# Kernel tuning notes

Hardware: AMD Instinct MI355X
Metric: run time of the kernel (lower is better)

## Reference

```python
import jax, jax.numpy as jnp
import numpy as np

N_HEAD = 16
D_HEAD = 64
D_MODEL = 1024
D_INNER = 4096
QLEN = 1024
MLEN = 1024
BSZ = 2
LN_EPS = 1e-5


def _layer_norm(x, g, b, eps=LN_EPS):
    mu = jnp.mean(x, axis=-1, keepdims=True)
    var = jnp.var(x, axis=-1, keepdims=True)
    return (x - mu) * jax.lax.rsqrt(var + eps) * g + b


def _rel_shift(x):
    # x: [qlen, rlen, bsz, n_head]
    q, r, b, n = x.shape
    zp = jnp.zeros((q, 1, b, n), x.dtype)
    xp = jnp.concatenate([zp, x], axis=1).reshape(r + 1, q, b, n)
    return xp[1:].reshape(q, r, b, n)


def setup_inputs() -> dict:
    key = jax.random.key(0)
    ks = jax.random.split(key, 12)
    klen = MLEN + QLEN
    w = jax.random.normal(ks[0], (QLEN, BSZ, D_MODEL), jnp.float32)
    r = jax.random.normal(ks[1], (klen, D_MODEL), jnp.float32)
    mems = jax.random.normal(ks[2], (MLEN, BSZ, D_MODEL), jnp.float32)
    # causal mask: query i attends keys j <= i + mlen
    i = jnp.arange(QLEN)[:, None]
    j = jnp.arange(klen)[None, :]
    attn_mask = (j > i + MLEN)[:, :, None]  # [qlen, klen, 1] bool
    s = 0.02
    params = dict(
        qkv_w=jax.random.normal(ks[3], (3 * N_HEAD * D_HEAD, D_MODEL), jnp.float32) * s,
        r_net_w=jax.random.normal(ks[4], (N_HEAD * D_HEAD, D_MODEL), jnp.float32) * s,
        o_w=jax.random.normal(ks[5], (D_MODEL, N_HEAD * D_HEAD), jnp.float32) * s,
        r_r_bias=jax.random.normal(ks[6], (N_HEAD, D_HEAD), jnp.float32) * s,
        r_w_bias=jax.random.normal(ks[7], (N_HEAD, D_HEAD), jnp.float32) * s,
        ln1_g=jnp.ones((D_MODEL,), jnp.float32),
        ln1_b=jnp.zeros((D_MODEL,), jnp.float32),
        ff_w1=jax.random.normal(ks[8], (D_INNER, D_MODEL), jnp.float32) * s,
        ff_b1=jnp.zeros((D_INNER,), jnp.float32),
        ff_w2=jax.random.normal(ks[9], (D_MODEL, D_INNER), jnp.float32) * s,
        ff_b2=jnp.zeros((D_MODEL,), jnp.float32),
        ln2_g=jnp.ones((D_MODEL,), jnp.float32),
        ln2_b=jnp.zeros((D_MODEL,), jnp.float32),
    )
    return dict(w=w, r=r, mems=mems, attn_mask=attn_mask, **params)


def reference(w, r, mems, attn_mask, qkv_w, r_net_w, o_w, r_r_bias, r_w_bias,
              ln1_g, ln1_b, ff_w1, ff_b1, ff_w2, ff_b2, ln2_g, ln2_b):
    qlen, bsz = w.shape[0], w.shape[1]
    scale = 1.0 / (D_HEAD ** 0.5)
    cat = jnp.concatenate([mems, w], axis=0)              # [klen, b, d_model]
    klen = cat.shape[0]
    w_heads = cat @ qkv_w.T                                # [klen, b, 3*n*d]
    wq, wk, wv = jnp.split(w_heads, 3, axis=-1)
    wq = wq[-qlen:]
    r_head_k = (r @ r_net_w.T).reshape(-1, N_HEAD, D_HEAD)  # [rlen, n, d]
    wq = wq.reshape(qlen, bsz, N_HEAD, D_HEAD)
    wk = wk.reshape(klen, bsz, N_HEAD, D_HEAD)
    wv = wv.reshape(klen, bsz, N_HEAD, D_HEAD)
    AC = jnp.einsum('ibnd,jbnd->ijbn', wq + r_w_bias, wk)   # content term
    BD = jnp.einsum('ibnd,jnd->ijbn', wq + r_r_bias, r_head_k)
    BD = _rel_shift(BD)                                     # position term
    attn_score = (AC + BD) * scale
    mask_value = jnp.finfo(attn_score.dtype).min
    attn_score = jnp.where(attn_mask[:, :, :, None], mask_value, attn_score)
    attn_prob = jax.nn.softmax(attn_score, axis=1)
    attn_vec = jnp.einsum('ijbn,jbnd->ibnd', attn_prob, wv)
    attn_vec = attn_vec.reshape(qlen, bsz, N_HEAD * D_HEAD)
    attn_out = attn_vec @ o_w.T
    h = _layer_norm(w + attn_out, ln1_g, ln1_b)             # post-lnorm
    core = jax.nn.relu(h @ ff_w1.T + ff_b1) @ ff_w2.T + ff_b2
    out = _layer_norm(h + core, ln2_g, ln2_b)
    return out
```

## Files before the change

kernel.cpp:

```cpp
#include <hip/hip_runtime.h>
#include <math.h>

#define QLEN 1024
#define MLEN 1024
#define KLEN 2048
#define BSZc 2
#define NH 16
#define DH 64
#define DM 1024
#define DI 4096

typedef unsigned short ushort_t;
typedef __attribute__((ext_vector_type(8))) short short8;
typedef __attribute__((ext_vector_type(4))) float f32x4;

__device__ __forceinline__ ushort_t f2bf(float x) {
    unsigned int u = __float_as_uint(x);
    unsigned int r = (u + 0x7FFFu + ((u >> 16) & 1u)) >> 16;
    return (ushort_t)r;
}

__device__ __forceinline__ void gload_lds16(const ushort_t* g, ushort_t* l) {
    __builtin_amdgcn_global_load_lds(
        (const __attribute__((address_space(1))) unsigned int*)g,
        (__attribute__((address_space(3))) unsigned int*)l,
        16, 0, 0);
}

__device__ __forceinline__ void cast8(const float* s, ushort_t* d, int g) {
    const float4 a = *(const float4*)(s + g * 8);
    const float4 b = *(const float4*)(s + g * 8 + 4);
    short8 o;
    o[0] = (short)f2bf(a.x); o[1] = (short)f2bf(a.y);
    o[2] = (short)f2bf(a.z); o[3] = (short)f2bf(a.w);
    o[4] = (short)f2bf(b.x); o[5] = (short)f2bf(b.y);
    o[6] = (short)f2bf(b.z); o[7] = (short)f2bf(b.w);
    *(short8*)(d + g * 8) = o;
}

__global__ __launch_bounds__(256)
void cast_phase1(const float* __restrict__ qkv_w, const float* __restrict__ rnet_w,
                 const float* __restrict__ mems, const float* __restrict__ w,
                 const float* __restrict__ r,
                 ushort_t* __restrict__ W1, ushort_t* __restrict__ W2,
                 ushort_t* __restrict__ Acat, ushort_t* __restrict__ Rsrc)
{
    int g = blockIdx.x * 256 + threadIdx.x;
    if (g < 393216)            { cast8(qkv_w,  W1,              g); }
    else if (g < 524288)       { cast8(rnet_w, W2,              g - 393216); }
    else if (g < 786432)       { cast8(mems,   Acat,            g - 524288); }
    else if (g < 1048576)      { cast8(w,      Acat + 2097152,  g - 786432); }
    else if (g < 1310720)      { cast8(r,      Rsrc,            g - 1048576); }
}

__global__ __launch_bounds__(256)
void cast_phase2(const float* __restrict__ o_w, const float* __restrict__ ffw1,
                 const float* __restrict__ ffw2,
                 ushort_t* __restrict__ W3, ushort_t* __restrict__ W4,
                 ushort_t* __restrict__ W5)
{
    int g = blockIdx.x * 256 + threadIdx.x;
    if (g < 131072)            { cast8(o_w,  W3, g); }
    else if (g < 655360)       { cast8(ffw1, W4, g - 131072); }
    else if (g < 1179648)      { cast8(ffw2, W5, g - 655360); }
}

template<int EMODE, int ACT, int BN, int SPLIT>
__global__ __launch_bounds__(256)
void gemm_mfma(const ushort_t* __restrict__ A, const ushort_t* __restrict__ B,
               const float* __restrict__ bias,
               void* __restrict__ O0v, void* __restrict__ O1v,
               int M, int N, int Ks, int lda, int ldb)
{
    constexpr int JT = BN / 32;
    __shared__ ushort_t At0[128 * 32];
    __shared__ ushort_t At1[128 * 32];
    __shared__ ushort_t Bt0[BN * 32];
    __shared__ ushort_t Bt1[BN * 32];

    const int tid  = threadIdx.x;
    const int lane = tid & 63;
    const int w    = tid >> 6;
    const int lr   = lane & 15;
    const int quad = lane >> 4;
    const int m0   = blockIdx.x * 128;
    const int n0   = blockIdx.y * BN;
    const int z    = (SPLIT > 1) ? (int)blockIdx.z : 0;
    const int kbase = z * Ks;
    const int wm0  = (w >> 1) * 64;
    const int wn0  = (w & 1) * (BN / 2);

    f32x4 acc[4][JT];
#pragma unroll
    for (int it = 0; it < 4; ++it)
#pragma unroll
        for (int jt = 0; jt < JT; ++jt) acc[it][jt] = (f32x4){0.f, 0.f, 0.f, 0.f};

    const int srow = lane >> 2;
    const int scol = (lane & 3) << 3;
    const ushort_t* Ag = A + (size_t)(m0 + w * 32 + srow) * lda + kbase + scol;
    ushort_t* a00 = At0 + (w * 32) * 32;
    ushort_t* a01 = At0 + (w * 32 + 16) * 32;
    ushort_t* a10 = At1 + (w * 32) * 32;
    ushort_t* a11 = At1 + (w * 32 + 16) * 32;
    const ushort_t* Bg;
    ushort_t *b00, *b01 = nullptr, *b10, *b11 = nullptr;
    if (BN == 128) {
        Bg  = B + (size_t)(n0 + w * 32 + srow) * ldb + kbase + scol;
        b00 = Bt0 + (w * 32) * 32;
        b01 = Bt0 + (w * 32 + 16) * 32;
        b10 = Bt1 + (w * 32) * 32;
        b11 = Bt1 + (w * 32 + 16) * 32;
    } else {
        Bg  = B + (size_t)(n0 + w * 16 + srow) * ldb + kbase + scol;
        b00 = Bt0 + (w * 16) * 32;
        b10 = Bt1 + (w * 16) * 32;
    }

    const ushort_t* Ato0 = At0 + (wm0 + lr) * 32 + quad * 8;
    const ushort_t* Ato1 = At1 + (wm0 + lr) * 32 + quad * 8;
    const ushort_t* Bto0 = Bt0 + (wn0 + lr) * 32 + quad * 8;
    const ushort_t* Bto1 = Bt1 + (wn0 + lr) * 32 + quad * 8;

    for (int k0 = 0; k0 < Ks; k0 += 64) {
        __syncthreads();
        gload_lds16(Ag + k0, a00);
        gload_lds16(Ag + (size_t)16 * lda + k0, a01);
        gload_lds16(Ag + k0 + 32, a10);
        gload_lds16(Ag + (size_t)16 * lda + k0 + 32, a11);
        if (BN == 128) {
            gload_lds16(Bg + k0, b00);
            gload_lds16(Bg + (size_t)16 * ldb + k0, b01);
            gload_lds16(Bg + k0 + 32, b10);
            gload_lds16(Bg + (size_t)16 * ldb + k0 + 32, b11);
        } else {
            gload_lds16(Bg + k0, b00);
            gload_lds16(Bg + k0 + 32, b10);
        }
        __syncthreads();

        short8 af[4], bf[JT];
#pragma unroll
        for (int it = 0; it < 4; ++it)
            af[it] = *(const short8*)(Ato0 + it * 16 * 32);
#pragma unroll
        for (int jt = 0; jt < JT; ++jt)
            bf[jt] = *(const short8*)(Bto0 + jt * 16 * 32);
#pragma unroll
        for (int it = 0; it < 4; ++it)
#pragma unroll
            for (int jt = 0; jt < JT; ++jt)
                acc[it][jt] = __builtin_amdgcn_mfma_f32_16x16x32_bf16(
                    af[it], bf[jt], acc[it][jt], 0, 0, 0);
#pragma unroll
        for (int it = 0; it < 4; ++it)
            af[it] = *(const short8*)(Ato1 + it * 16 * 32);
#pragma unroll
        for (int jt = 0; jt < JT; ++jt)
            bf[jt] = *(const short8*)(Bto1 + jt * 16 * 32);
#pragma unroll
        for (int it = 0; it < 4; ++it)
#pragma unroll
            for (int jt = 0; jt < JT; ++jt)
                acc[it][jt] = __builtin_amdgcn_mfma_f32_16x16x32_bf16(
                    af[it], bf[jt], acc[it][jt], 0, 0, 0);
    }

#pragma unroll
    for (int it = 0; it < 4; ++it)
#pragma unroll
        for (int jt = 0; jt < JT; ++jt)
#pragma unroll
            for (int rg = 0; rg < 4; ++rg) {
                const int m = m0 + wm0 + it * 16 + quad * 4 + rg;
                const int n = n0 + wn0 + jt * 16 + lr;
                float v = acc[it][jt][rg];
                if (EMODE == 0) {
                    float* dst = (float*)(z ? O1v : O0v);
                    if (bias && z == 0) v += bias[n];
                    dst[(size_t)m * N + n] = v;
                } else {
                    v += bias[n];
                    if (ACT == 1) v = fmaxf(v, 0.f);
                    ((ushort_t*)O0v)[(size_t)m * N + n] = f2bf(v);
                }
            }
}

__global__ __launch_bounds__(256)
void gemm_qkvr(const ushort_t* __restrict__ Acat, const ushort_t* __restrict__ W1,
               const ushort_t* __restrict__ Rsrc, const ushort_t* __restrict__ W2,
               ushort_t* __restrict__ Qac, ushort_t* __restrict__ Qbd,
               ushort_t* __restrict__ Kbf, ushort_t* __restrict__ Vtb,
               ushort_t* __restrict__ Rh,
               const float* __restrict__ rwb, const float* __restrict__ rrb)
{
    __shared__ ushort_t At[128 * 32];
    __shared__ ushort_t Bt[128 * 32];

    const int bid  = blockIdx.x;
    const bool isr = bid >= 768;
    const ushort_t* A; const ushort_t* B; int m0, n0;
    if (!isr) { A = Acat; B = W1; m0 = (bid & 31) * 128; n0 = (bid >> 5) * 128; }
    else { int t = bid - 768; A = Rsrc; B = W2; m0 = (t & 15) * 128; n0 = (t >> 4) * 128; }
    const int K = 1024;

    const int tid  = threadIdx.x;
    const int lane = tid & 63;
    const int w    = tid >> 6;
    const int lr   = lane & 15;
    const int quad = lane >> 4;
    const int wm0  = (w >> 1) * 64;
    const int wn0  = (w & 1) * 64;

    f32x4 acc[4][4];
#pragma unroll
    for (int it = 0; it < 4; ++it)
#pragma unroll
        for (int jt = 0; jt < 4; ++jt) acc[it][jt] = (f32x4){0.f, 0.f, 0.f, 0.f};

    const int srow = lane >> 2;
    const int scol = (lane & 3) << 3;
    const ushort_t* Ag = A + (size_t)(m0 + w * 32 + srow) * K + scol;
    const ushort_t* Bg = B + (size_t)(n0 + w * 32 + srow) * K + scol;
    ushort_t* lA0 = At + (w * 32) * 32;
    ushort_t* lA1 = At + (w * 32 + 16) * 32;
    ushort_t* lB0 = Bt + (w * 32) * 32;
    ushort_t* lB1 = Bt + (w * 32 + 16) * 32;

    const ushort_t* Ato = At + (wm0 + lr) * 32 + quad * 8;
    const ushort_t* Bto = Bt + (wn0 + lr) * 32 + quad * 8;

    for (int k0 = 0; k0 < K; k0 += 32) {
        __syncthreads();
        gload_lds16(Ag + k0, lA0);
        gload_lds16(Ag + (size_t)16 * K + k0, lA1);
        gload_lds16(Bg + k0, lB0);
        gload_lds16(Bg + (size_t)16 * K + k0, lB1);
        __syncthreads();

        short8 af[4], bf[4];
#pragma unroll
        for (int it = 0; it < 4; ++it)
            af[it] = *(const short8*)(Ato + it * 16 * 32);
#pragma unroll
        for (int jt = 0; jt < 4; ++jt)
            bf[jt] = *(const short8*)(Bto + jt * 16 * 32);
#pragma unroll
        for (int it = 0; it < 4; ++it)
#pragma unroll
            for (int jt = 0; jt < 4; ++jt)
                acc[it][jt] = __builtin_amdgcn_mfma_f32_16x16x32_bf16(
                    af[it], bf[jt], acc[it][jt], 0, 0, 0);
    }

#pragma unroll
    for (int it = 0; it < 4; ++it)
#pragma unroll
        for (int jt = 0; jt < 4; ++jt)
#pragma unroll
            for (int rg = 0; rg < 4; ++rg) {
                const int m = m0 + wm0 + it * 16 + quad * 4 + rg;
                const int n = n0 + wn0 + jt * 16 + lr;
                const float v = acc[it][jt][rg];
                if (!isr) {
                    const int j = m >> 1, b = m & 1;
                    const int part = n >> 10, hh = (n >> 6) & 15, d = n & 63;
                    if (part == 0) {
                        if (j >= MLEN) {
                            const int qi = j - MLEN;
                            const size_t qidx = (((size_t)(b * NH + hh)) * QLEN + qi) * DH + d;
                            Qac[qidx] = f2bf(v + rwb[hh * DH + d]);
                            Qbd[qidx] = f2bf(v + rrb[hh * DH + d]);
                        }
                    } else if (part == 1) {
                        Kbf[(((size_t)(b * NH + hh)) * KLEN + j) * DH + d] = f2bf(v);
                    } else {
                        Vtb[(((size_t)(b * NH + hh)) * DH + d) * KLEN + j] = f2bf(v);
                    }
                } else {
                    const int hh = n >> 6, d = n & 63;
                    Rh[(((size_t)hh) * KLEN + m) * DH + d] = f2bf(v);
                }
            }
}

__global__ __launch_bounds__(256, 4)
void attn_mfma(const ushort_t* __restrict__ Qac, const ushort_t* __restrict__ Qbd,
               const ushort_t* __restrict__ Kb, const ushort_t* __restrict__ Vt,
               const ushort_t* __restrict__ Rb,
               float* __restrict__ Op0, float* __restrict__ Op1,
               float* __restrict__ Mp, float* __restrict__ Lp)
{
    __shared__ ushort_t Rt[128][72];
    __shared__ float    Bw[4][16][84];

    const int tid  = threadIdx.x;
    const int lane = tid & 63;
    const int w    = tid >> 6;
    const int lr   = lane & 15;
    const int quad = lane >> 4;
    const int qt   = blockIdx.x;
    const int s    = blockIdx.y;
    const int bh   = blockIdx.z;
    const int i0   = qt << 6;
    const int h    = bh & 15;
    const int b    = bh >> 4;

    short8 qaf[2], qbf[2];
    {
        const size_t rowoff = ((size_t)bh * QLEN + i0 + w * 16 + lr) * DH;
#pragma unroll
        for (int kt = 0; kt < 2; ++kt) {
            qaf[kt] = *(const short8*)(Qac + rowoff + kt * 32 + quad * 8);
            qbf[kt] = *(const short8*)(Qbd + rowoff + kt * 32 + quad * 8);
        }
    }

    f32x4 O[4];
#pragma unroll
    for (int nt = 0; nt < 4; ++nt) O[nt] = (f32x4){0.f, 0.f, 0.f, 0.f};
    float m_run = -3.4e38f, l_run = 0.f;

    const int nc  = qt + 17;
    const int stw = 3 - w;
    const float SC = 0.125f * 1.44269504f;
    const ushort_t* Kh = Kb + (size_t)bh * KLEN * DH;
    const ushort_t* Vh = Vt + (size_t)bh * DH * KLEN;
    const ushort_t* Rhp = Rb + (size_t)h * KLEN * DH;

    for (int c = s; c < nc; c += 2) {
        const int j0 = c << 6;
        const int wb = 960 - i0 + j0;
        __syncthreads();
#pragma unroll
        for (int t = 0; t < 4; ++t) {
            int f = tid + (t << 8);
            int rl2 = f >> 3, c8 = (f & 7) << 3;
            int g = wb + rl2;
            int gc = g > (KLEN - 1) ? (KLEN - 1) : g;
            *(int4*)&Rt[rl2][c8] = *(const int4*)(Rhp + (size_t)gc * DH + c8);
        }
        __syncthreads();

#pragma unroll
        for (int ctl = 0; ctl < 5; ++ctl) {
            const int wr = (stw + ctl) * 16 + lr;
            f32x4 z = (f32x4){0.f, 0.f, 0.f, 0.f};
#pragma unroll
            for (int kt = 0; kt < 2; ++kt) {
                short8 rb2 = *(const short8*)&Rt[wr][kt * 32 + quad * 8];
                z = __builtin_amdgcn_mfma_f32_16x16x32_bf16(qbf[kt], rb2, z, 0, 0, 0);
            }
#pragma unroll
            for (int rg = 0; rg < 4; ++rg)
                Bw[w][quad * 4 + rg][ctl * 16 + lr] = z[rg];
        }
#pragma unroll
        for (int ct = 0; ct < 4; ++ct) {
            f32x4 z = (f32x4){0.f, 0.f, 0.f, 0.f};
#pragma unroll
            for (int kt = 0; kt < 2; ++kt) {
                short8 kb2 = *(const short8*)(Kh + (size_t)(j0 + ct * 16 + lr) * DH + kt * 32 + quad * 8);
                z = __builtin_amdgcn_mfma_f32_16x16x32_bf16(qaf[kt], kb2, z, 0, 0, 0);
            }
#pragma unroll
            for (int rg = 0; rg < 4; ++rg) {
                const int rrow = quad * 4 + rg;
                Bw[w][rrow][ct * 16 + lr + 15 - rrow] += z[rg];
            }
        }

        const int lim = i0 + w * 16 + lr + 1024 - j0;
        float pv[16];
        float mx = -3.4e38f;
#pragma unroll
        for (int kt = 0; kt < 2; ++kt)
#pragma unroll
            for (int t = 0; t < 8; ++t) {
                const int jj = kt * 32 + quad * 8 + t;
                float sv = Bw[w][lr][jj + 15 - lr] * SC;
                sv = (jj > lim) ? -3.4e38f : sv;
                pv[kt * 8 + t] = sv;
                mx = fmaxf(mx, sv);
            }
        mx = fmaxf(mx, __shfl_xor(mx, 16, 64));
        mx = fmaxf(mx, __shfl_xor(mx, 32, 64));
        const float m_new = fmaxf(m_run, mx);
        float ps = 0.f;
        short8 pf[2];
#pragma unroll
        for (int kt = 0; kt < 2; ++kt)
#pragma unroll
            for (int t = 0; t < 8; ++t) {
                const float e = exp2f(pv[kt * 8 + t] - m_new);
                ps += e;
                pf[kt][t] = (short)f2bf(e);
            }
        ps += __shfl_xor(ps, 16, 64);
        ps += __shfl_xor(ps, 32, 64);
        const float alpha = exp2f(m_run - m_new);
        m_run = m_new;
        l_run = l_run * alpha + ps;

        float ar[4];
#pragma unroll
        for (int rg = 0; rg < 4; ++rg)
            ar[rg] = __shfl(alpha, quad * 4 + rg, 64);
#pragma unroll
        for (int nt = 0; nt < 4; ++nt) {
            O[nt][0] *= ar[0]; O[nt][1] *= ar[1];
            O[nt][2] *= ar[2]; O[nt][3] *= ar[3];
        }
#pragma unroll
        for (int kt = 0; kt < 2; ++kt)
#pragma unroll
            for (int nt = 0; nt < 4; ++nt) {
                short8 vb = *(const short8*)(Vh + (size_t)(nt * 16 + lr) * KLEN + j0 + kt * 32 + quad * 8);
                O[nt] = __builtin_amdgcn_mfma_f32_16x16x32_bf16(pf[kt], vb, O[nt], 0, 0, 0);
            }
    }

    if (quad == 0) {
        const size_t mi = ((size_t)s * 32 + bh) * QLEN + i0 + w * 16 + lr;
        Mp[mi] = m_run;
        Lp[mi] = l_run;
    }
    float* Op = s ? Op1 : Op0;
#pragma unroll
    for (int nt = 0; nt < 4; ++nt)
#pragma unroll
        for (int rg = 0; rg < 4; ++rg) {
            const int i = i0 + w * 16 + quad * 4 + rg;
            Op[((size_t)i * BSZc + b) * DM + h * DH + nt * 16 + lr] = O[nt][rg];
        }
}

__global__ __launch_bounds__(256)
void attn_merge(const float* __restrict__ O0, const float* __restrict__ O1,
                const float* __restrict__ Mp, const float* __restrict__ Lp,
                ushort_t* __restrict__ AV)
{
    const int row = blockIdx.x;
    const int tid = threadIdx.x;
    const int i = row >> 1, b = row & 1;
    const int h = tid >> 4;
    const int bh = b * NH + h;
    const size_t mi = (size_t)bh * QLEN + i;
    const float m1 = Mp[mi],             l1 = Lp[mi];
    const float m2 = Mp[32 * QLEN + mi], l2 = Lp[32 * QLEN + mi];
    const float M = fmaxf(m1, m2);
    const float a1 = exp2f(m1 - M), a2 = exp2f(m2 - M);
    const float rl = 1.f / (l1 * a1 + l2 * a2);
    const float f1 = a1 * rl, f2 = a2 * rl;
    const float4 o1 = ((const float4*)(O0 + (size_t)row * DM))[tid];
    const float4 o2 = ((const float4*)(O1 + (size_t)row * DM))[tid];
    ushort_t* p = AV + (size_t)row * DM + tid * 4;
    p[0] = f2bf(o1.x * f1 + o2.x * f2);
    p[1] = f2bf(o1.y * f1 + o2.y * f2);
    p[2] = f2bf(o1.z * f1 + o2.z * f2);
    p[3] = f2bf(o1.w * f1 + o2.w * f2);
}

__global__ __launch_bounds__(256)
void add_ln(const float* __restrict__ X, const float* __restrict__ Y0,
            const float* __restrict__ Y1,
            const float* __restrict__ gg, const float* __restrict__ bb,
            float* __restrict__ out, ushort_t* __restrict__ outb)
{
    const int row  = blockIdx.x;
    const int tid  = threadIdx.x;
    const int lane = tid & 63;
    const int w    = tid >> 6;
    __shared__ float ssum[4], ssq[4];

    const float4 xv = ((const float4*)(X + (size_t)row * DM))[tid];
    const float4 yv = ((const float4*)(Y0 + (size_t)row * DM))[tid];
    float v0 = xv.x + yv.x, v1 = xv.y + yv.y;
    float v2 = xv.z + yv.z, v3 = xv.w + yv.w;
    if (Y1) {
        const float4 zv = ((const float4*)(Y1 + (size_t)row * DM))[tid];
        v0 += zv.x; v1 += zv.y; v2 += zv.z; v3 += zv.w;
    }
    float s = v0 + v1 + v2 + v3;
    float q = v0 * v0 + v1 * v1 + v2 * v2 + v3 * v3;
#pragma unroll
    for (int off = 32; off > 0; off >>= 1) {
        s += __shfl_xor(s, off, 64);
        q += __shfl_xor(q, off, 64);
    }
    if (lane == 0) { ssum[w] = s; ssq[w] = q; }
    __syncthreads();
    s = ssum[0] + ssum[1] + ssum[2] + ssum[3];
    q = ssq[0] + ssq[1] + ssq[2] + ssq[3];
    const float mean = s * (1.f / DM);
    const float var  = q * (1.f / DM) - mean * mean;
    const float rs   = rsqrtf(var + 1e-5f);
    const float4 g4 = ((const float4*)gg)[tid];
    const float4 b4 = ((const float4*)bb)[tid];
    float4 ov;
    ov.x = (v0 - mean) * rs * g4.x + b4.x;
    ov.y = (v1 - mean) * rs * g4.y + b4.y;
    ov.z = (v2 - mean) * rs * g4.z + b4.z;
    ov.w = (v3 - mean) * rs * g4.w + b4.w;
    ((float4*)(out + (size_t)row * DM))[tid] = ov;
    if (outb) {
        ushort_t* p = outb + (size_t)row * DM + tid * 4;
        p[0] = f2bf(ov.x); p[1] = f2bf(ov.y);
        p[2] = f2bf(ov.z); p[3] = f2bf(ov.w);
    }
}

extern "C" void kernel_launch(void* const* d_in, const int* in_sizes, int n_in,
                              void* d_out, int out_size, void* d_ws, size_t ws_size,
                              hipStream_t stream)
{
    (void)in_sizes; (void)n_in; (void)out_size; (void)ws_size;
    const float* w      = (const float*)d_in[0];
    const float* r      = (const float*)d_in[1];
    const float* mems   = (const float*)d_in[2];
    const float* qkv_w  = (const float*)d_in[4];
    const float* rnet_w = (const float*)d_in[5];
    const float* o_w    = (const float*)d_in[6];
    const float* r_r_b  = (const float*)d_in[7];
    const float* r_w_b  = (const float*)d_in[8];
    const float* ln1g   = (const float*)d_in[9];
    const float* ln1b   = (const float*)d_in[10];
    const float* ffw1   = (const float*)d_in[11];
    const float* ffb1   = (const float*)d_in[12];
    const float* ffw2   = (const float*)d_in[13];
    const float* ffb2   = (const float*)d_in[14];
    const float* ln2g   = (const float*)d_in[15];
    const float* ln2b   = (const float*)d_in[16];
    float* out = (float*)d_out;

    char* wsb = (char*)d_ws;
    const size_t MB = 1024 * 1024;
    ushort_t* W1    = (ushort_t*)(wsb + 0 * MB);
    ushort_t* W2    = (ushort_t*)(wsb + 6 * MB);
    ushort_t* Acat  = (ushort_t*)(wsb + 8 * MB);
    ushort_t* Rsrc  = (ushort_t*)(wsb + 16 * MB);
    ushort_t* Qac   = (ushort_t*)(wsb + 20 * MB);
    ushort_t* Qbd   = (ushort_t*)(wsb + 24 * MB);
    ushort_t* Kbf   = (ushort_t*)(wsb + 28 * MB);
    ushort_t* Vt    = (ushort_t*)(wsb + 36 * MB);
    ushort_t* Rh    = (ushort_t*)(wsb + 44 * MB);
    float*    Op0   = (float*)(wsb + 48 * MB);
    float*    Op1   = (float*)(wsb + 56 * MB);
    float*    Mp    = (float*)(wsb + 4 * MB);
    float*    Lp    = (float*)(wsb + 4 * MB + 512 * 1024);
    ushort_t* AVec  = (ushort_t*)(wsb + 0 * MB);
    ushort_t* W3    = (ushort_t*)(wsb + 4 * MB);
    float*    AOut0 = (float*)(wsb + 8 * MB);
    float*    AOut1 = (float*)(wsb + 44 * MB);
    float*    Hbuf  = (float*)(wsb + 16 * MB);
    ushort_t* Hbf   = (ushort_t*)(wsb + 24 * MB);
    ushort_t* W4    = (ushort_t*)(wsb + 28 * MB);
    ushort_t* FFbf  = (ushort_t*)(wsb + 36 * MB);
    ushort_t* W5    = (ushort_t*)(wsb + 52 * MB);
    float*    Core0 = (float*)(wsb + 0 * MB);
    float*    Core1 = (float*)(wsb + 8 * MB);

    dim3 blk(256);

    cast_phase1<<<dim3(5120), blk, 0, stream>>>(qkv_w, rnet_w, mems, w, r,
                                                W1, W2, Acat, Rsrc);

    gemm_qkvr<<<dim3(896), blk, 0, stream>>>(
        Acat, W1, Rsrc, W2, Qac, Qbd, Kbf, Vt, Rh, r_w_b, r_r_b);

    attn_mfma<<<dim3(16, 2, 32), blk, 0, stream>>>(
        Qac, Qbd, Kbf, Vt, Rh, Op0, Op1, Mp, Lp);

    attn_merge<<<dim3(2048), blk, 0, stream>>>(Op0, Op1, Mp, Lp, AVec);

    cast_phase2<<<dim3(4608), blk, 0, stream>>>(o_w, ffw1, ffw2, W3, W4, W5);

    gemm_mfma<0, 0, 64, 2><<<dim3(16, 16, 2), blk, 0, stream>>>(
        AVec, W3, nullptr, AOut0, AOut1, 2048, 1024, 512, 1024, 1024);

    add_ln<<<dim3(2 * QLEN), blk, 0, stream>>>(w, AOut0, AOut1, ln1g, ln1b, Hbuf, Hbf);

    gemm_mfma<3, 1, 128, 1><<<dim3(16, 32), blk, 0, stream>>>(
        Hbf, W4, ffb1, FFbf, nullptr, 2048, 4096, 1024, 1024, 1024);

    gemm_mfma<0, 0, 64, 2><<<dim3(16, 16, 2), blk, 0, stream>>>(
        FFbf, W5, ffb2, Core0, Core1, 2048, 1024, 2048, 4096, 4096);

    add_ln<<<dim3(2 * QLEN), blk, 0, stream>>>(Hbuf, Core0, Core1, ln2g, ln2b, out, nullptr);
}
```

Baseline: 437.2 us.

## Stage K and V tiles in LDS and reuse R rows via ring buffer

The attention kernel now loads K and V tiles cooperatively into shared memory instead of having each wave read them directly from global memory. Each split block now processes a contiguous range of key chunks rather than alternating ones. That lets consecutive iterations reuse half of the relative-position R tile through a 128-row ring buffer, so only 64 new rows are loaded per step. The V tile aliases the score scratch buffer, which adds extra barriers per iteration, and the occupancy hint drops from 4 to 3 blocks per CU to fit the larger LDS footprint.

```diff
diff --git a/kernel.cpp b/kernel.cpp
--- a/kernel.cpp
+++ b/kernel.cpp
@@ -285,15 +285,17 @@
             }
 }
 
-__global__ __launch_bounds__(256, 4)
+__global__ __launch_bounds__(256, 3)
 void attn_mfma(const ushort_t* __restrict__ Qac, const ushort_t* __restrict__ Qbd,
                const ushort_t* __restrict__ Kb, const ushort_t* __restrict__ Vt,
                const ushort_t* __restrict__ Rb,
                float* __restrict__ Op0, float* __restrict__ Op1,
                float* __restrict__ Mp, float* __restrict__ Lp)
 {
-    __shared__ ushort_t Rt[128][72];
-    __shared__ float    Bw[4][16][84];
+    __shared__ __align__(16) ushort_t Kt[64 * 72];
+    __shared__ __align__(16) ushort_t Rt[128 * 72];
+    __shared__ __align__(16) float    Bw[4][16][84];
+    ushort_t* Vl = (ushort_t*)&Bw[0][0][0];
 
     const int tid  = threadIdx.x;
     const int lane = tid & 63;
@@ -322,34 +324,55 @@
     for (int nt = 0; nt < 4; ++nt) O[nt] = (f32x4){0.f, 0.f, 0.f, 0.f};
     float m_run = -3.4e38f, l_run = 0.f;
 
-    const int nc  = qt + 17;
-    const int stw = 3 - w;
+    const int nc   = qt + 17;
+    const int half = (nc + 1) >> 1;
+    const int c_lo = s ? half : 0;
+    const int c_hi = s ? nc : half;
+    const int stw  = 3 - w;
     const float SC = 0.125f * 1.44269504f;
-    const ushort_t* Kh = Kb + (size_t)bh * KLEN * DH;
-    const ushort_t* Vh = Vt + (size_t)bh * DH * KLEN;
+    const ushort_t* Kh  = Kb + (size_t)bh * KLEN * DH;
+    const ushort_t* Vh  = Vt + (size_t)bh * DH * KLEN;
     const ushort_t* Rhp = Rb + (size_t)h * KLEN * DH;
 
-    for (int c = s; c < nc; c += 2) {
+    for (int c = c_lo; c < c_hi; ++c) {
         const int j0 = c << 6;
         const int wb = 960 - i0 + j0;
-        __syncthreads();
-#pragma unroll
-        for (int t = 0; t < 4; ++t) {
+
+#pragma unroll
+        for (int t = 0; t < 2; ++t) {
             int f = tid + (t << 8);
-            int rl2 = f >> 3, c8 = (f & 7) << 3;
-            int g = wb + rl2;
-            int gc = g > (KLEN - 1) ? (KLEN - 1) : g;
-            *(int4*)&Rt[rl2][c8] = *(const int4*)(Rhp + (size_t)gc * DH + c8);
+            int row = f >> 3, c8 = (f & 7) << 3;
+            *(int4*)&Kt[row * 72 + c8] = *(const int4*)(Kh + (size_t)(j0 + row) * DH + c8);
+        }
+        if (c == c_lo) {
+#pragma unroll
+            for (int t = 0; t < 4; ++t) {
+                int f = tid + (t << 8);
+                int rl2 = f >> 3, c8 = (f & 7) << 3;
+                int g = wb + rl2;
+                int gc = g > (KLEN - 1) ? (KLEN - 1) : g;
+                *(int4*)&Rt[((g) & 127) * 72 + c8] = *(const int4*)(Rhp + (size_t)gc * DH + c8);
+            }
+        } else {
+#pragma unroll
+            for (int t = 0; t < 2; ++t) {
+                int f = tid + (t << 8);
+                int rl2 = (f >> 3) + 64, c8 = (f & 7) << 3;
+                int g = wb + rl2;
+                int gc = g > (KLEN - 1) ? (KLEN - 1) : g;
+                *(int4*)&Rt[((g) & 127) * 72 + c8] = *(const int4*)(Rhp + (size_t)gc * DH + c8);
+            }
         }
         __syncthreads();
 
 #pragma unroll
         for (int ctl = 0; ctl < 5; ++ctl) {
             const int wr = (stw + ctl) * 16 + lr;
+            const int ring = (wb + wr) & 127;
             f32x4 z = (f32x4){0.f, 0.f, 0.f, 0.f};
 #pragma unroll
             for (int kt = 0; kt < 2; ++kt) {
-                short8 rb2 = *(const short8*)&Rt[wr][kt * 32 + quad * 8];
+                short8 rb2 = *(const short8*)&Rt[ring * 72 + kt * 32 + quad * 8];
                 z = __builtin_amdgcn_mfma_f32_16x16x32_bf16(qbf[kt], rb2, z, 0, 0, 0);
             }
 #pragma unroll
@@ -361,7 +384,7 @@
             f32x4 z = (f32x4){0.f, 0.f, 0.f, 0.f};
 #pragma unroll
             for (int kt = 0; kt < 2; ++kt) {
-                short8 kb2 = *(const short8*)(Kh + (size_t)(j0 + ct * 16 + lr) * DH + kt * 32 + quad * 8);
+                short8 kb2 = *(const short8*)&Kt[(ct * 16 + lr) * 72 + kt * 32 + quad * 8];
                 z = __builtin_amdgcn_mfma_f32_16x16x32_bf16(qaf[kt], kb2, z, 0, 0, 0);
             }
 #pragma unroll
@@ -403,6 +426,16 @@
         m_run = m_new;
         l_run = l_run * alpha + ps;
 
+        __syncthreads();
+
+#pragma unroll
+        for (int t = 0; t < 2; ++t) {
+            int f = tid + (t << 8);
+            int d = f >> 3, c8 = (f & 7) << 3;
+            *(int4*)&Vl[d * 72 + c8] = *(const int4*)(Vh + (size_t)d * KLEN + j0 + c8);
+        }
+        __syncthreads();
+
         float ar[4];
 #pragma unroll
         for (int rg = 0; rg < 4; ++rg)
@@ -416,7 +449,7 @@
         for (int kt = 0; kt < 2; ++kt)
 #pragma unroll
             for (int nt = 0; nt < 4; ++nt) {
-                short8 vb = *(const short8*)(Vh + (size_t)(nt * 16 + lr) * KLEN + j0 + kt * 32 + quad * 8);
+                short8 vb = *(const short8*)&Vl[(nt * 16 + lr) * 72 + kt * 32 + quad * 8];
                 O[nt] = __builtin_amdgcn_mfma_f32_16x16x32_bf16(pf[kt], vb, O[nt], 0, 0, 0);
             }
     }
```

Result: faster. 397.2 us (-9.1%).
